# Performance work log

Hardware: AMD Instinct MI355X
Metric: run time of the kernel (lower is better)

Reference implementation:

```python
import jax, jax.numpy as jnp
import numpy as np

N_NODES = 50000
N_EDGES = 800000
IN_DIM = 128
HEADS1, D1 = 4, 16   # hidden_dim // 4 = 16, concat -> 64
HID = HEADS1 * D1    # 64
OUT_DIM = 40
NEG_SLOPE = 0.2      # PyG GATConv default


def setup_inputs() -> dict:
    key = jax.random.key(0)
    ks = jax.random.split(key, 11)
    x = jax.random.normal(ks[0], (N_NODES, IN_DIM), dtype=jnp.float32)
    edge_index = jax.random.randint(ks[1], (2, N_EDGES), 0, N_NODES)
    s1 = 1.0 / np.sqrt(IN_DIM)
    s2 = 1.0 / np.sqrt(HID)
    return {
        "x": x,
        "edge_index": edge_index,
        "W1": jax.random.normal(ks[2], (IN_DIM, HEADS1 * D1), dtype=jnp.float32) * s1,
        "a_src1": jax.random.normal(ks[3], (HEADS1, D1), dtype=jnp.float32) * s2,
        "a_dst1": jax.random.normal(ks[4], (HEADS1, D1), dtype=jnp.float32) * s2,
        "b1": jnp.zeros((HID,), dtype=jnp.float32),
        "W2": jax.random.normal(ks[5], (HID, OUT_DIM), dtype=jnp.float32) * s2,
        "a_src2": jax.random.normal(ks[6], (1, OUT_DIM), dtype=jnp.float32) * s2,
        "a_dst2": jax.random.normal(ks[7], (1, OUT_DIM), dtype=jnp.float32) * s2,
        "b2": jnp.zeros((OUT_DIM,), dtype=jnp.float32),
    }


def gat_conv(x, src, dst, W, a_src, a_dst, b, heads, d, n_nodes):
    # linear projection, split into heads: [N, H, d]
    h = (x @ W).reshape(n_nodes, heads, d)
    # per-node attention logits: [N, H]
    alpha_src = jnp.einsum("nhd,hd->nh", h, a_src)
    alpha_dst = jnp.einsum("nhd,hd->nh", h, a_dst)
    # edge attention coefficients
    e = jax.nn.leaky_relu(alpha_src[src] + alpha_dst[dst], NEG_SLOPE)  # [E, H]
    # segment softmax over incoming edges of each destination node
    e_max = jax.ops.segment_max(e, dst, num_segments=n_nodes)
    e_max = jnp.where(jnp.isfinite(e_max), e_max, 0.0)
    e_exp = jnp.exp(e - e_max[dst])
    denom = jax.ops.segment_sum(e_exp, dst, num_segments=n_nodes)
    alpha = e_exp / (denom[dst] + 1e-16)  # [E, H]
    # weighted scatter-aggregate of source messages
    out = jax.ops.segment_sum(h[src] * alpha[..., None], dst, num_segments=n_nodes)
    return out.reshape(n_nodes, heads * d) + b


def reference(x, edge_index, W1, a_src1, a_dst1, b1, W2, a_src2, a_dst2, b2):
    n = x.shape[0]
    # PyG GATConv add_self_loops=True
    loop = jnp.arange(n, dtype=edge_index.dtype)
    src = jnp.concatenate([edge_index[0], loop])
    dst = jnp.concatenate([edge_index[1], loop])
    h = jax.nn.relu(gat_conv(x, src, dst, W1, a_src1, a_dst1, b1, HEADS1, D1, n))
    # dropout is identity in eval mode
    h = gat_conv(h, src, dst, W2, a_src2, a_dst2, b2, 1, OUT_DIM, n)
    return jax.nn.log_softmax(h, axis=1)
```

## Files before the change

kernel.cpp:

```cpp
#include <hip/hip_runtime.h>
#include <hip/hip_fp16.h>
#include <math.h>

#define NN    50000
#define NE0   800000
#define NE    850000
#define INDIM 128
#define HID   64
#define OUTD  40

#define NB    391
#define BSH   7
#define BCAP  3072

__global__ __launch_bounds__(256) void k_bin(const int* __restrict__ ei,
                                             int* __restrict__ bcur,
                                             unsigned int* __restrict__ epack) {
    __shared__ int lh[NB];
    __shared__ int lbase[NB];
    __shared__ unsigned ebuf[3328];
    const int tid = threadIdx.x;
    const int CH = (NE + 255) / 256;
    const int e0 = blockIdx.x * CH;
    const int e1 = (e0 + CH < NE) ? e0 + CH : NE;
    const int cnt = e1 - e0;

    for (int i = tid; i < NB; i += 256) lh[i] = 0;
    __syncthreads();
    for (int i = tid; i < cnt; i += 256) {
        int e = e0 + i;
        int src, dst;
        if (e < NE0) { src = ei[e]; dst = ei[NE0 + e]; }
        else         { src = e - NE0; dst = src; }
        int bkt = dst >> BSH;
        ebuf[i] = (unsigned)src | ((unsigned)(dst & 127) << 16) | ((unsigned)bkt << 23);
        atomicAdd(&lh[bkt], 1);
    }
    __syncthreads();
    for (int i = tid; i < NB; i += 256) {
        int c = lh[i];
        lbase[i] = c ? (i * BCAP + atomicAdd(&bcur[i], c)) : 0;
        lh[i] = 0;
    }
    __syncthreads();
    for (int i = tid; i < cnt; i += 256) {
        unsigned rec = ebuf[i];
        int bkt = rec >> 23;
        int lpos = atomicAdd(&lh[bkt], 1);
        epack[lbase[bkt] + lpos] = rec & 0x7FFFFFu;
    }
}

union __align__(16) SMu {
    struct { float Wl[INDIM * HID]; float xs[64 * 132]; } g;
    struct { int lh[128]; int lcur[128]; int sblk; } c;
};

__global__ __launch_bounds__(256, 2) void k_g1csr(
    const float* __restrict__ x, const float* __restrict__ W1,
    const float* __restrict__ a_s, const float* __restrict__ a_d,
    __half* __restrict__ h1h, float* __restrict__ asrc1, float* __restrict__ adst1,
    const int* __restrict__ bcur, const unsigned int* __restrict__ epack,
    int* __restrict__ off_s, int* __restrict__ off_e, int* __restrict__ esrc)
{
    __shared__ SMu sm;
    const int tid = threadIdx.x;

    if (blockIdx.x < NB) {
        const int lane = tid & 63;
        const int b = blockIdx.x;
        const int e0 = b * BCAP;
        const int cnt = bcur[b];

        if (tid < 128) sm.c.lh[tid] = 0;
        __syncthreads();
        for (int i = tid; i < cnt; i += 256)
            atomicAdd(&sm.c.lh[epack[e0 + i] >> 16], 1);
        __syncthreads();

        int v = 0, incl = 0;
        if (tid < 128) {
            v = sm.c.lh[tid];
            incl = v;
#pragma unroll
            for (int s = 1; s < 64; s <<= 1) {
                int t = __shfl_up(incl, s);
                if (lane >= s) incl += t;
            }
        }
        if (tid == 63) sm.c.sblk = incl;
        __syncthreads();
        if (tid >= 64 && tid < 128) incl += sm.c.sblk;
        if (tid < 128) {
            int ex = e0 + incl - v;
            sm.c.lcur[tid] = ex;
            int gd = b * 128 + tid;
            if (gd < NN) { off_s[gd] = ex; off_e[gd] = ex + v; }
        }
        __syncthreads();

        for (int i = tid; i < cnt; i += 256) {
            unsigned int p = epack[e0 + i];
            int pos = atomicAdd(&sm.c.lcur[p >> 16], 1);
            esrc[pos] = (int)(p & 0xFFFFu);
        }
        return;
    }

    const int r0 = (blockIdx.x - NB) * 64;

    const float4* W4 = (const float4*)W1;
    float4* Wl4 = (float4*)sm.g.Wl;
#pragma unroll
    for (int i = 0; i < 8; ++i) Wl4[tid + i * 256] = W4[tid + i * 256];

    const float4* x4 = (const float4*)x;
#pragma unroll
    for (int i = 0; i < 8; ++i) {
        int idx = tid + i * 256;
        int row = idx >> 5;
        int k4  = idx & 31;
        int nr = r0 + row;
        float4 v = make_float4(0.f, 0.f, 0.f, 0.f);
        if (nr < NN) v = x4[(size_t)nr * 32 + k4];
        *(float4*)&sm.g.xs[row * 132 + k4 * 4] = v;
    }
    __syncthreads();

    const int rg = tid >> 4;
    const int cg = tid & 15;
    const int c4 = cg * 4;
    const float as0 = a_s[c4], as1v = a_s[c4+1], as2v = a_s[c4+2], as3v = a_s[c4+3];
    const float ad0 = a_d[c4], ad1v = a_d[c4+1], ad2v = a_d[c4+2], ad3v = a_d[c4+3];

    float acc[4][4];
#pragma unroll
    for (int i = 0; i < 4; ++i)
#pragma unroll
        for (int j = 0; j < 4; ++j) acc[i][j] = 0.f;

#pragma unroll 4
    for (int k4 = 0; k4 < 32; ++k4) {
        float4 xv[4];
#pragma unroll
        for (int i = 0; i < 4; ++i)
            xv[i] = *(const float4*)&sm.g.xs[(rg * 4 + i) * 132 + k4 * 4];
        const float* wp = &sm.g.Wl[(k4 * 4) * HID + c4];
        float4 w0 = *(const float4*)(wp);
        float4 w1 = *(const float4*)(wp + HID);
        float4 w2 = *(const float4*)(wp + 2 * HID);
        float4 w3 = *(const float4*)(wp + 3 * HID);
#pragma unroll
        for (int i = 0; i < 4; ++i) {
            acc[i][0] += xv[i].x * w0.x + xv[i].y * w1.x + xv[i].z * w2.x + xv[i].w * w3.x;
            acc[i][1] += xv[i].x * w0.y + xv[i].y * w1.y + xv[i].z * w2.y + xv[i].w * w3.y;
            acc[i][2] += xv[i].x * w0.z + xv[i].y * w1.z + xv[i].z * w2.z + xv[i].w * w3.z;
            acc[i][3] += xv[i].x * w0.w + xv[i].y * w1.w + xv[i].z * w2.w + xv[i].w * w3.w;
        }
    }

#pragma unroll
    for (int i = 0; i < 4; ++i) {
        const int n = r0 + rg * 4 + i;
        if (n < NN) {
            __half2 ha = __floats2half2_rn(acc[i][0], acc[i][1]);
            __half2 hb = __floats2half2_rn(acc[i][2], acc[i][3]);
            *(__half2*)&h1h[(size_t)n * HID + c4]     = ha;
            *(__half2*)&h1h[(size_t)n * HID + c4 + 2] = hb;
        }
        float ps = acc[i][0] * as0 + acc[i][1] * as1v + acc[i][2] * as2v + acc[i][3] * as3v;
        float pd = acc[i][0] * ad0 + acc[i][1] * ad1v + acc[i][2] * ad2v + acc[i][3] * ad3v;
        ps += __shfl_xor(ps, 1); ps += __shfl_xor(ps, 2);
        pd += __shfl_xor(pd, 1); pd += __shfl_xor(pd, 2);
        if ((cg & 3) == 0 && n < NN) {
            int head = cg >> 2;
            asrc1[n * 4 + head] = ps;
            adst1[n * 4 + head] = pd;
        }
    }
}

__global__ __launch_bounds__(256) void k_fagg1g2(
    const int* __restrict__ off_s, const int* __restrict__ off_e,
    const int* __restrict__ esrc, const float* __restrict__ asrc1,
    const float* __restrict__ adst1,
    const __half* __restrict__ h1h, const float* __restrict__ b1,
    const float* __restrict__ W2, const float* __restrict__ a_s2,
    const float* __restrict__ a_d2,
    __half* __restrict__ h2h, float* __restrict__ asrc2, float* __restrict__ adst2)
{
    __shared__ __align__(16) float W2l[HID * OUTD];
    __shared__ __align__(16) float hml[16][72];
    __shared__ float s_a2s[OUTD], s_a2d[OUTD];
    __shared__ float s_ps[16], s_pd[16];
    const int tid = threadIdx.x;

    {
        const float4* W24 = (const float4*)W2;
        float4* W2l4 = (float4*)W2l;
        for (int i = tid; i < (HID * OUTD) / 4; i += 256) W2l4[i] = W24[i];
        if (tid < OUTD) { s_a2s[tid] = a_s2[tid]; s_a2d[tid] = a_d2[tid]; }
        if (tid < 16)   { s_ps[tid] = 0.f; s_pd[tid] = 0.f; }
    }

    const int wv = tid >> 6, lane = tid & 63;
    const int g = lane >> 4, li = lane & 15;
    const int r = wv * 4 + g;
    const int n = blockIdx.x * 16 + r;
    const int s0 = off_s[n], s1 = off_e[n];
    const int hp = li >> 2;
    const float adst = adst1[n * 4 + hp];
    const int last = (s1 > 0) ? s1 - 1 : 0;

    float l = 0.f, a0 = 0.f, a1 = 0.f, a2 = 0.f, a3 = 0.f;
    const char* hb = (const char*)h1h;

    int sxA[8];
#pragma unroll
    for (int j = 0; j < 8; ++j) {
        int ix = s0 + j;
        sxA[j] = esrc[ix < s1 ? ix : last];
    }
    for (int t = s0; t < s1; t += 8) {
        float ax[8];
#pragma unroll
        for (int j = 0; j < 8; ++j) ax[j] = asrc1[sxA[j] * 4 + hp];
        uint2 raw[8];
#pragma unroll
        for (int j = 0; j < 8; ++j)
            raw[j] = *(const uint2*)(hb + ((size_t)sxA[j] * 128 + li * 8));
        int sxB[8];
        const int t2 = t + 8;
#pragma unroll
        for (int j = 0; j < 8; ++j) {
            int ix = t2 + j;
            sxB[j] = esrc[ix < s1 ? ix : last];
        }
#pragma unroll
        for (int j = 0; j < 8; ++j) {
            float e = ax[j] + adst;
            e = (e > 0.f) ? e : 0.2f * e;
            float w = __expf(e);
            w = ((t + j) < s1) ? w : 0.f;
            float2 f0 = __half22float2(*(__half2*)&raw[j].x);
            float2 f1 = __half22float2(*(__half2*)&raw[j].y);
            l  += w;
            a0 += w * f0.x;
            a1 += w * f0.y;
            a2 += w * f1.x;
            a3 += w * f1.y;
        }
#pragma unroll
        for (int j = 0; j < 8; ++j) sxA[j] = sxB[j];
    }

    {
        float rcp = 1.f / l;
        float4 bv = *(const float4*)&b1[li * 4];
        float o0 = fmaxf(a0 * rcp + bv.x, 0.f);
        float o1 = fmaxf(a1 * rcp + bv.y, 0.f);
        float o2 = fmaxf(a2 * rcp + bv.z, 0.f);
        float o3 = fmaxf(a3 * rcp + bv.w, 0.f);
        *(float4*)&hml[r][li * 4] = make_float4(o0, o1, o2, o3);
    }
    __syncthreads();

    if (tid < 160) {
        const int rr = tid / 10;
        const int c4 = (tid - rr * 10) * 4;
        float4 acc = make_float4(0.f, 0.f, 0.f, 0.f);
#pragma unroll 4
        for (int k4 = 0; k4 < 16; ++k4) {
            float4 hv = *(const float4*)&hml[rr][k4 * 4];
            const float* wp = &W2l[(k4 * 4) * OUTD + c4];
            float4 w0 = *(const float4*)(wp);
            float4 w1 = *(const float4*)(wp + OUTD);
            float4 w2 = *(const float4*)(wp + 2 * OUTD);
            float4 w3 = *(const float4*)(wp + 3 * OUTD);
            acc.x += hv.x * w0.x + hv.y * w1.x + hv.z * w2.x + hv.w * w3.x;
            acc.y += hv.x * w0.y + hv.y * w1.y + hv.z * w2.y + hv.w * w3.y;
            acc.z += hv.x * w0.z + hv.y * w1.z + hv.z * w2.z + hv.w * w3.z;
            acc.w += hv.x * w0.w + hv.y * w1.w + hv.z * w2.w + hv.w * w3.w;
        }
        const int n2 = blockIdx.x * 16 + rr;
        __half2 ha = __floats2half2_rn(acc.x, acc.y);
        __half2 hc = __floats2half2_rn(acc.z, acc.w);
        uint2 st;
        st.x = *(unsigned*)&ha;
        st.y = *(unsigned*)&hc;
        *(uint2*)((char*)h2h + ((size_t)n2 * 80 + c4 * 2)) = st;
        float ps = acc.x * s_a2s[c4] + acc.y * s_a2s[c4 + 1] + acc.z * s_a2s[c4 + 2] + acc.w * s_a2s[c4 + 3];
        float pd = acc.x * s_a2d[c4] + acc.y * s_a2d[c4 + 1] + acc.z * s_a2d[c4 + 2] + acc.w * s_a2d[c4 + 3];
        atomicAdd(&s_ps[rr], ps);
        atomicAdd(&s_pd[rr], pd);
    }
    __syncthreads();
    if (tid < 16) {
        const int n2 = blockIdx.x * 16 + tid;
        asrc2[n2] = s_ps[tid];
        adst2[n2] = s_pd[tid];
    }
}

__global__ __launch_bounds__(256) void k_fagg2(
    const int* __restrict__ off_s, const int* __restrict__ off_e,
    const int* __restrict__ esrc, const float* __restrict__ asrc2,
    const float* __restrict__ adst2,
    const __half* __restrict__ h2h, const float* __restrict__ b2,
    float* __restrict__ out)
{
    __shared__ float svals[24][OUTD];
    const int wv = threadIdx.x >> 6, lane = threadIdx.x & 63;
    const int g = lane / 10;
    const int li = lane - g * 10;
    const bool ga = (g < 6);
    const int n = blockIdx.x * 24 + wv * 6 + (ga ? g : 0);
    const bool valid = ga && (n < NN);
    const int s0 = valid ? off_s[n] : 0;
    const int s1 = valid ? off_e[n] : 0;
    const float adst = valid ? adst2[n] : 0.f;
    const int last = (s1 > 0) ? s1 - 1 : 0;

    float l = 0.f, a0 = 0.f, a1 = 0.f, a2 = 0.f, a3 = 0.f;
    const char* hb = (const char*)h2h;

    int sxA[8];
#pragma unroll
    for (int j = 0; j < 8; ++j) {
        int ix = s0 + j;
        sxA[j] = esrc[ix < s1 ? ix : last];
    }
    for (int t = s0; t < s1; t += 8) {
        float ax[8];
#pragma unroll
        for (int j = 0; j < 8; ++j) ax[j] = asrc2[sxA[j]];
        uint2 raw[8];
#pragma unroll
        for (int j = 0; j < 8; ++j)
            raw[j] = *(const uint2*)(hb + ((size_t)sxA[j] * 80 + li * 8));
        int sxB[8];
        const int t2 = t + 8;
#pragma unroll
        for (int j = 0; j < 8; ++j) {
            int ix = t2 + j;
            sxB[j] = esrc[ix < s1 ? ix : last];
        }
#pragma unroll
        for (int j = 0; j < 8; ++j) {
            float e = ax[j] + adst;
            e = (e > 0.f) ? e : 0.2f * e;
            float w = __expf(e);
            w = ((t + j) < s1) ? w : 0.f;
            float2 f0 = __half22float2(*(__half2*)&raw[j].x);
            float2 f1 = __half22float2(*(__half2*)&raw[j].y);
            l  += w;
            a0 += w * f0.x;
            a1 += w * f0.y;
            a2 += w * f1.x;
            a3 += w * f1.y;
        }
#pragma unroll
        for (int j = 0; j < 8; ++j) sxA[j] = sxB[j];
    }
    if (valid) {
        float rcp = 1.f / l;
        float4 bv = *(const float4*)&b2[li * 4];
        int r = wv * 6 + g;
        svals[r][li * 4]     = a0 * rcp + bv.x;
        svals[r][li * 4 + 1] = a1 * rcp + bv.y;
        svals[r][li * 4 + 2] = a2 * rcp + bv.z;
        svals[r][li * 4 + 3] = a3 * rcp + bv.w;
    }
    __syncthreads();

    for (int r = wv; r < 24; r += 4) {
        int n2 = blockIdx.x * 24 + r;
        if (n2 >= NN) continue;
        float v = (lane < OUTD) ? svals[r][lane] : -1e30f;
        float mx = v;
#pragma unroll
        for (int o = 32; o; o >>= 1) mx = fmaxf(mx, __shfl_xor(mx, o));
        float ex = (lane < OUTD) ? __expf(v - mx) : 0.f;
        float sm = ex;
#pragma unroll
        for (int o = 32; o; o >>= 1) sm += __shfl_xor(sm, o);
        if (lane < OUTD) out[(size_t)n2 * OUTD + lane] = v - mx - __logf(sm);
    }
}

extern "C" void kernel_launch(void* const* d_in, const int* in_sizes, int n_in,
                              void* d_out, int out_size, void* d_ws, size_t ws_size,
                              hipStream_t stream)
{
    const float* x   = (const float*)d_in[0];
    const int*   ei  = (const int*)  d_in[1];
    const float* W1  = (const float*)d_in[2];
    const float* as1 = (const float*)d_in[3];
    const float* ad1 = (const float*)d_in[4];
    const float* b1  = (const float*)d_in[5];
    const float* W2  = (const float*)d_in[6];
    const float* as2 = (const float*)d_in[7];
    const float* ad2 = (const float*)d_in[8];
    const float* b2  = (const float*)d_in[9];
    float* out = (float*)d_out;

    char* ws = (char*)d_ws;
    __half* h1h   = (__half*)(ws);
    __half* h2h   = (__half*)(ws + 12800000);
    float*  asrc1 = (float*) (ws + 16800000);
    float*  adst1 = (float*) (ws + 17600000);
    float*  asrc2 = (float*) (ws + 18400000);
    float*  adst2 = (float*) (ws + 18600000);
    int*    off_s = (int*)   (ws + 18800000);
    int*    off_e = (int*)   (ws + 19000000);
    unsigned int* epack = (unsigned int*)(ws + 19200000);
    int*    esrc  = (int*)   (ws + 24004608);
    int*    bcur  = (int*)   (ws + 28809216);

    hipMemsetAsync(bcur, 0, NB * sizeof(int), stream);
    hipLaunchKernelGGL(k_bin,     dim3(256),      dim3(256), 0, stream, ei, bcur, epack);
    hipLaunchKernelGGL(k_g1csr,   dim3(NB + 782), dim3(256), 0, stream,
                       x, W1, as1, ad1, h1h, asrc1, adst1, bcur, epack, off_s, off_e, esrc);
    hipLaunchKernelGGL(k_fagg1g2, dim3(3125),     dim3(256), 0, stream,
                       off_s, off_e, esrc, asrc1, adst1, h1h, b1, W2, as2, ad2, h2h, asrc2, adst2);
    hipLaunchKernelGGL(k_fagg2,   dim3(2084),     dim3(256), 0, stream,
                       off_s, off_e, esrc, asrc2, adst2, h2h, b2, out);
}
```

Measured before the change: 184.6 us.

## Fuse edge binning with layer-1 GEMM and store CSR sources as 16-bit

Moves the edge-binning work into the same launch as the layer-1 projection GEMM, so binning blocks run alongside GEMM blocks, and splits the CSR build into its own kernel. The fused kernel uses 256 binning blocks plus 782 GEMM blocks, 1038 in total. Source indices in the CSR array are stored as u16 instead of int, which halves the bytes read during both aggregation passes. The workspace offsets are compacted to match. The 16-bit index relies on NN being at most 65536, and the `last` clamp now assumes every node has at least one edge, which the self-loops guarantee.

```diff
diff --git a/kernel.cpp b/kernel.cpp
--- a/kernel.cpp
+++ b/kernel.cpp
@@ -13,101 +13,56 @@
 #define BSH   7
 #define BCAP  3072
 
-__global__ __launch_bounds__(256) void k_bin(const int* __restrict__ ei,
-                                             int* __restrict__ bcur,
-                                             unsigned int* __restrict__ epack) {
-    __shared__ int lh[NB];
-    __shared__ int lbase[NB];
-    __shared__ unsigned ebuf[3328];
-    const int tid = threadIdx.x;
-    const int CH = (NE + 255) / 256;
-    const int e0 = blockIdx.x * CH;
-    const int e1 = (e0 + CH < NE) ? e0 + CH : NE;
-    const int cnt = e1 - e0;
-
-    for (int i = tid; i < NB; i += 256) lh[i] = 0;
-    __syncthreads();
-    for (int i = tid; i < cnt; i += 256) {
-        int e = e0 + i;
-        int src, dst;
-        if (e < NE0) { src = ei[e]; dst = ei[NE0 + e]; }
-        else         { src = e - NE0; dst = src; }
-        int bkt = dst >> BSH;
-        ebuf[i] = (unsigned)src | ((unsigned)(dst & 127) << 16) | ((unsigned)bkt << 23);
-        atomicAdd(&lh[bkt], 1);
-    }
-    __syncthreads();
-    for (int i = tid; i < NB; i += 256) {
-        int c = lh[i];
-        lbase[i] = c ? (i * BCAP + atomicAdd(&bcur[i], c)) : 0;
-        lh[i] = 0;
-    }
-    __syncthreads();
-    for (int i = tid; i < cnt; i += 256) {
-        unsigned rec = ebuf[i];
-        int bkt = rec >> 23;
-        int lpos = atomicAdd(&lh[bkt], 1);
-        epack[lbase[bkt] + lpos] = rec & 0x7FFFFFu;
-    }
-}
-
-union __align__(16) SMu {
+typedef unsigned short u16;
+
+union __align__(16) SMa {
     struct { float Wl[INDIM * HID]; float xs[64 * 132]; } g;
-    struct { int lh[128]; int lcur[128]; int sblk; } c;
+    struct { int lh[NB]; int lbase[NB]; unsigned ebuf[3328]; } b;
 };
 
-__global__ __launch_bounds__(256, 2) void k_g1csr(
+__global__ __launch_bounds__(256, 2) void k_binG1(
+    const int* __restrict__ ei, int* __restrict__ bcur, unsigned int* __restrict__ epack,
     const float* __restrict__ x, const float* __restrict__ W1,
     const float* __restrict__ a_s, const float* __restrict__ a_d,
-    __half* __restrict__ h1h, float* __restrict__ asrc1, float* __restrict__ adst1,
-    const int* __restrict__ bcur, const unsigned int* __restrict__ epack,
-    int* __restrict__ off_s, int* __restrict__ off_e, int* __restrict__ esrc)
+    __half* __restrict__ h1h, float* __restrict__ asrc1, float* __restrict__ adst1)
 {
-    __shared__ SMu sm;
+    __shared__ SMa sm;
     const int tid = threadIdx.x;
 
-    if (blockIdx.x < NB) {
-        const int lane = tid & 63;
-        const int b = blockIdx.x;
-        const int e0 = b * BCAP;
-        const int cnt = bcur[b];
-
-        if (tid < 128) sm.c.lh[tid] = 0;
+    if (blockIdx.x < 256) {
+        const int CH = (NE + 255) / 256;
+        const int e0 = blockIdx.x * CH;
+        const int e1 = (e0 + CH < NE) ? e0 + CH : NE;
+        const int cnt = e1 - e0;
+
+        for (int i = tid; i < NB; i += 256) sm.b.lh[i] = 0;
         __syncthreads();
-        for (int i = tid; i < cnt; i += 256)
-            atomicAdd(&sm.c.lh[epack[e0 + i] >> 16], 1);
+        for (int i = tid; i < cnt; i += 256) {
+            int e = e0 + i;
+            int src, dst;
+            if (e < NE0) { src = ei[e]; dst = ei[NE0 + e]; }
+            else         { src = e - NE0; dst = src; }
+            int bkt = dst >> BSH;
+            sm.b.ebuf[i] = (unsigned)src | ((unsigned)(dst & 127) << 16) | ((unsigned)bkt << 23);
+            atomicAdd(&sm.b.lh[bkt], 1);
+        }
         __syncthreads();
-
-        int v = 0, incl = 0;
-        if (tid < 128) {
-            v = sm.c.lh[tid];
-            incl = v;
-#pragma unroll
-            for (int s = 1; s < 64; s <<= 1) {
-                int t = __shfl_up(incl, s);
-                if (lane >= s) incl += t;
-            }
-        }
-        if (tid == 63) sm.c.sblk = incl;
+        for (int i = tid; i < NB; i += 256) {
+            int c = sm.b.lh[i];
+            sm.b.lbase[i] = c ? (i * BCAP + atomicAdd(&bcur[i], c)) : 0;
+            sm.b.lh[i] = 0;
+        }
         __syncthreads();
-        if (tid >= 64 && tid < 128) incl += sm.c.sblk;
-        if (tid < 128) {
-            int ex = e0 + incl - v;
-            sm.c.lcur[tid] = ex;
-            int gd = b * 128 + tid;
-            if (gd < NN) { off_s[gd] = ex; off_e[gd] = ex + v; }
-        }
-        __syncthreads();
-
         for (int i = tid; i < cnt; i += 256) {
-            unsigned int p = epack[e0 + i];
-            int pos = atomicAdd(&sm.c.lcur[p >> 16], 1);
-            esrc[pos] = (int)(p & 0xFFFFu);
+            unsigned rec = sm.b.ebuf[i];
+            int bkt = rec >> 23;
+            int lpos = atomicAdd(&sm.b.lh[bkt], 1);
+            epack[sm.b.lbase[bkt] + lpos] = rec & 0x7FFFFFu;
         }
         return;
     }
 
-    const int r0 = (blockIdx.x - NB) * 64;
+    const int r0 = (blockIdx.x - 256) * 64;
 
     const float4* W4 = (const float4*)W1;
     float4* Wl4 = (float4*)sm.g.Wl;
@@ -180,9 +135,55 @@
     }
 }
 
+__global__ __launch_bounds__(256) void k_csr(
+    const int* __restrict__ bcur, const unsigned int* __restrict__ epack,
+    int* __restrict__ off_s, int* __restrict__ off_e, u16* __restrict__ esrc)
+{
+    __shared__ int lh[128];
+    __shared__ int lcur[128];
+    __shared__ int sblk;
+    const int tid = threadIdx.x, lane = tid & 63;
+    const int b = blockIdx.x;
+    const int e0 = b * BCAP;
+    const int cnt = bcur[b];
+
+    if (tid < 128) lh[tid] = 0;
+    __syncthreads();
+    for (int i = tid; i < cnt; i += 256)
+        atomicAdd(&lh[epack[e0 + i] >> 16], 1);
+    __syncthreads();
+
+    int v = 0, incl = 0;
+    if (tid < 128) {
+        v = lh[tid];
+        incl = v;
+#pragma unroll
+        for (int s = 1; s < 64; s <<= 1) {
+            int t = __shfl_up(incl, s);
+            if (lane >= s) incl += t;
+        }
+    }
+    if (tid == 63) sblk = incl;
+    __syncthreads();
+    if (tid >= 64 && tid < 128) incl += sblk;
+    if (tid < 128) {
+        int ex = e0 + incl - v;
+        lcur[tid] = ex;
+        int gd = b * 128 + tid;
+        if (gd < NN) { off_s[gd] = ex; off_e[gd] = ex + v; }
+    }
+    __syncthreads();
+
+    for (int i = tid; i < cnt; i += 256) {
+        unsigned int p = epack[e0 + i];
+        int pos = atomicAdd(&lcur[p >> 16], 1);
+        esrc[pos] = (u16)(p & 0xFFFFu);
+    }
+}
+
 __global__ __launch_bounds__(256) void k_fagg1g2(
     const int* __restrict__ off_s, const int* __restrict__ off_e,
-    const int* __restrict__ esrc, const float* __restrict__ asrc1,
+    const u16* __restrict__ esrc, const float* __restrict__ asrc1,
     const float* __restrict__ adst1,
     const __half* __restrict__ h1h, const float* __restrict__ b1,
     const float* __restrict__ W2, const float* __restrict__ a_s2,
@@ -210,7 +211,7 @@
     const int s0 = off_s[n], s1 = off_e[n];
     const int hp = li >> 2;
     const float adst = adst1[n * 4 + hp];
-    const int last = (s1 > 0) ? s1 - 1 : 0;
+    const int last = s1 - 1;
 
     float l = 0.f, a0 = 0.f, a1 = 0.f, a2 = 0.f, a3 = 0.f;
     const char* hb = (const char*)h1h;
@@ -304,7 +305,7 @@
 
 __global__ __launch_bounds__(256) void k_fagg2(
     const int* __restrict__ off_s, const int* __restrict__ off_e,
-    const int* __restrict__ esrc, const float* __restrict__ asrc2,
+    const u16* __restrict__ esrc, const float* __restrict__ asrc2,
     const float* __restrict__ adst2,
     const __half* __restrict__ h2h, const float* __restrict__ b2,
     float* __restrict__ out)
@@ -406,23 +407,24 @@
 
     char* ws = (char*)d_ws;
     __half* h1h   = (__half*)(ws);
-    __half* h2h   = (__half*)(ws + 12800000);
-    float*  asrc1 = (float*) (ws + 16800000);
-    float*  adst1 = (float*) (ws + 17600000);
-    float*  asrc2 = (float*) (ws + 18400000);
-    float*  adst2 = (float*) (ws + 18600000);
-    int*    off_s = (int*)   (ws + 18800000);
-    int*    off_e = (int*)   (ws + 19000000);
-    unsigned int* epack = (unsigned int*)(ws + 19200000);
-    int*    esrc  = (int*)   (ws + 24004608);
-    int*    bcur  = (int*)   (ws + 28809216);
+    __half* h2h   = (__half*)(ws +  6400000);
+    float*  asrc1 = (float*) (ws + 10400000);
+    float*  adst1 = (float*) (ws + 11200000);
+    float*  asrc2 = (float*) (ws + 12000000);
+    float*  adst2 = (float*) (ws + 12200000);
+    int*    off_s = (int*)   (ws + 12400000);
+    int*    off_e = (int*)   (ws + 12600000);
+    unsigned int* epack = (unsigned int*)(ws + 12800000);
+    u16*    esrc  = (u16*)   (ws + 17604608);
+    int*    bcur  = (int*)   (ws + 20006912);
 
     hipMemsetAsync(bcur, 0, NB * sizeof(int), stream);
-    hipLaunchKernelGGL(k_bin,     dim3(256),      dim3(256), 0, stream, ei, bcur, epack);
-    hipLaunchKernelGGL(k_g1csr,   dim3(NB + 782), dim3(256), 0, stream,
-                       x, W1, as1, ad1, h1h, asrc1, adst1, bcur, epack, off_s, off_e, esrc);
-    hipLaunchKernelGGL(k_fagg1g2, dim3(3125),     dim3(256), 0, stream,
+    hipLaunchKernelGGL(k_binG1,  dim3(1038), dim3(256), 0, stream,
+                       ei, bcur, epack, x, W1, as1, ad1, h1h, asrc1, adst1);
+    hipLaunchKernelGGL(k_csr,    dim3(NB),   dim3(256), 0, stream,
+                       bcur, epack, off_s, off_e, esrc);
+    hipLaunchKernelGGL(k_fagg1g2, dim3(3125), dim3(256), 0, stream,
                        off_s, off_e, esrc, asrc1, adst1, h1h, b1, W2, as2, ad2, h2h, asrc2, adst2);
-    hipLaunchKernelGGL(k_fagg2,   dim3(2084),     dim3(256), 0, stream,
+    hipLaunchKernelGGL(k_fagg2,  dim3(2084), dim3(256), 0, stream,
                        off_s, off_e, esrc, asrc2, adst2, h2h, b2, out);
 }
```

Measured after the change: 182.4 us. Within noise of the previous version (-1.2%).
